# Performance work log

Hardware: AMD Instinct MI355X
Metric: run time of the kernel (lower is better)

## Reference

```python
import jax, jax.numpy as jnp
import numpy as np

HEADS = 8
EPS = 1e-6
LN_EPS = 1e-5


def avg_pool(x, k):
    b, c, h, w = x.shape
    return x.reshape(b, c, h // k, k, w // k, k).mean(axis=(3, 5))


def layernorm(x, g, b):
    mu = x.mean(-1, keepdims=True)
    var = x.var(-1, keepdims=True)
    return (x - mu) / jnp.sqrt(var + LN_EPS) * g + b


def pos_embed_2d(h, w, c):
    # original calls build_2d_sincos_position_embedding(w=h, h=w): grid over (h, w), row-major flatten
    gw, gh = jnp.meshgrid(jnp.arange(h, dtype=jnp.float32),
                          jnp.arange(w, dtype=jnp.float32), indexing='ij')
    pd = c // 4
    omega = 1.0 / (10000.0 ** (jnp.arange(pd, dtype=jnp.float32) / pd))
    ow = gw.reshape(-1, 1) * omega  # (h*w, pd)
    oh = gh.reshape(-1, 1) * omega
    return jnp.concatenate([jnp.sin(ow), jnp.cos(ow), jnp.sin(oh), jnp.cos(oh)], axis=1)  # (h*w, c)


def _forward(a3, a4, q_w, q_b, q_ln_g, q_ln_b, k_w, k_b, k_ln_g, k_ln_b,
             v_w, v_b, out_w, out_b, lin1_w, lin1_b, lin2_w, lin2_b,
             n1_g, n1_b, n2_g, n2_b, idx):
    orig_a3 = a3
    if idx == 2:
        a3d = avg_pool(a3, 2)
    else:
        a3d = avg_pool(a3, 4)
        a4 = avg_pool(a4, 2)
    bs, c, h, w = a3d.shape
    L = h * w  # tgt_len == src_len (a3_down and a4 have equal spatial size)
    hd = c // HEADS

    residual = a3d.reshape(bs, c, L).transpose(0, 2, 1)  # (b, L, c)
    x3 = residual
    x4 = a4.reshape(bs, c, L).transpose(0, 2, 1)
    pos = pos_embed_2d(h, w, c)  # (L, c)
    x3 = x3 + pos[None]
    x4 = x4 + pos[None]

    Q = layernorm(x3 @ q_w + q_b, q_ln_g, q_ln_b)
    K = layernorm(x4 @ k_w + k_b, k_ln_g, k_ln_b)
    V = x4 @ v_w + v_b
    Q = jax.nn.relu(Q).reshape(bs, L, HEADS, hd).transpose(0, 2, 1, 3)  # (b,h,L,d)
    K = jax.nn.relu(K).reshape(bs, L, HEADS, hd).transpose(0, 2, 1, 3)
    V = V.reshape(bs, L, HEADS, hd).transpose(0, 2, 1, 3)

    # cosFormer position reweighting: index = pi/2 * (1..m) / m
    m = L
    wi = (np.pi / 2.0) * jnp.arange(1, m + 1, dtype=jnp.float32) / m  # (m,)
    sn = jnp.sin(wi)[None, None, :, None]
    cs = jnp.cos(wi)[None, None, :, None]
    Q_ = jnp.concatenate([Q * sn, Q * cs], axis=-1)  # (b,h,L,2d)
    K_ = jnp.concatenate([K * sn, K * cs], axis=-1)

    KV = jnp.einsum('bhld,bhlm->bhdm', K_, V)                     # (b,h,2d,d)
    Z = 1.0 / jnp.maximum(jnp.einsum('bhld,bhd->bhl', Q_, K_.sum(axis=2)), EPS)
    attn = jnp.einsum('bhld,bhdm->bhlm', Q_, KV) * Z[..., None]   # (b,h,L,d)
    attn = attn.transpose(0, 2, 1, 3).reshape(bs, L, c)

    out = attn @ out_w + out_b
    out = layernorm(out, n1_g, n1_b)     # normalize_before=False -> norm1 applied
    out = residual + out                 # dropout=0
    res2 = out
    out = jax.nn.gelu(out @ lin1_w + lin1_b, approximate=False) @ lin2_w + lin2_b
    out = layernorm(out, n2_g, n2_b)
    out = res2 + out

    a3sa = out.transpose(0, 2, 1).reshape(bs, c, h, w)
    a3sa = jax.image.resize(a3sa, orig_a3.shape, method='bilinear')  # align_corners=False
    return a3sa * orig_a3


def setup_inputs() -> dict:
    key = jax.random.key(0)
    ks = jax.random.split(key, 10)
    B, C = 16, 256
    C4 = 4 * C

    def w(k, shp):
        return jax.random.normal(k, shp, dtype=jnp.float32) * 0.02

    return {
        'a3': jax.random.normal(ks[0], (B, C, 128, 128), dtype=jnp.float32),
        'a4': jax.random.normal(ks[1], (B, C, 64, 64), dtype=jnp.float32),
        'q_w': w(ks[2], (C, C)), 'q_b': jnp.zeros((C,), jnp.float32),
        'q_ln_g': jnp.ones((C,), jnp.float32), 'q_ln_b': jnp.zeros((C,), jnp.float32),
        'k_w': w(ks[3], (C, C)), 'k_b': jnp.zeros((C,), jnp.float32),
        'k_ln_g': jnp.ones((C,), jnp.float32), 'k_ln_b': jnp.zeros((C,), jnp.float32),
        'v_w': w(ks[4], (C, C)), 'v_b': jnp.zeros((C,), jnp.float32),
        'out_w': w(ks[5], (C, C)), 'out_b': jnp.zeros((C,), jnp.float32),
        'lin1_w': w(ks[6], (C, C4)), 'lin1_b': jnp.zeros((C4,), jnp.float32),
        'lin2_w': w(ks[7], (C4, C)), 'lin2_b': jnp.zeros((C,), jnp.float32),
        'n1_g': jnp.ones((C,), jnp.float32), 'n1_b': jnp.zeros((C,), jnp.float32),
        'n2_g': jnp.ones((C,), jnp.float32), 'n2_b': jnp.zeros((C,), jnp.float32),
        'idx': 2,
    }


def reference(a3, a4, q_w, q_b, q_ln_g, q_ln_b, k_w, k_b, k_ln_g, k_ln_b,
              v_w, v_b, out_w, out_b, lin1_w, lin1_b, lin2_w, lin2_b,
              n1_g, n1_b, n2_g, n2_b, idx):
    return _forward(a3, a4, q_w, q_b, q_ln_g, q_ln_b, k_w, k_b, k_ln_g, k_ln_b,
                    v_w, v_b, out_w, out_b, lin1_w, lin1_b, lin2_w, lin2_b,
                    n1_g, n1_b, n2_g, n2_b, idx)
```

## Files before the change

### kernel.cpp

```cpp
#include <hip/hip_runtime.h>
#include <hip/hip_bf16.h>
#include <math.h>

#define HEADS 8
#define LL 4096
#define CDIM 256
#define BATCH 16
#define NROWS (BATCH*LL)

typedef __attribute__((ext_vector_type(8))) __bf16 bf16x8;
typedef __attribute__((ext_vector_type(4))) float f32x4;

__device__ inline float b2f(ushort u) {
    union { unsigned u; float f; } v; v.u = ((unsigned)u) << 16; return v.f;
}
__device__ inline ushort f2b(float f) {
    union { float f; unsigned u; } v; v.f = f;
    unsigned r = (v.u + 0x7FFF + ((v.u >> 16) & 1)) >> 16;
    return (ushort)r;
}
__device__ inline void gload16(const void* g, void* l) {
    __builtin_amdgcn_global_load_lds(
        (const __attribute__((address_space(1))) unsigned int*)g,
        (__attribute__((address_space(3))) unsigned int*)l, 16, 0, 0);
}

__global__ __launch_bounds__(256) void prep_kernel(
    float* __restrict__ pos, float* __restrict__ snc,
    const float* __restrict__ q_w, const float* __restrict__ k_w,
    const float* __restrict__ v_w, const float* __restrict__ o_w,
    const float* __restrict__ w1, const float* __restrict__ w2,
    ushort* __restrict__ wqT, ushort* __restrict__ wkT,
    ushort* __restrict__ wvT, ushort* __restrict__ woT,
    ushort* __restrict__ w1T, ushort* __restrict__ w2T)
{
    __shared__ float t[32][33];
    int bid = blockIdx.x;
    int tid = threadIdx.x;
    if (bid < 1024) {
        int c = tid;
        int k = c & 63;
        float omega = expf(-(float)k * (9.210340371976184f / 64.0f));
        #pragma unroll
        for (int i = 0; i < 4; ++i) {
            int l = bid * 4 + i;
            int y = l >> 6, x = l & 63;
            float coord = (c < 128) ? (float)y : (float)x;
            float ang = coord * omega;
            float val = ((c & 127) < 64) ? sinf(ang) : cosf(ang);
            pos[l * CDIM + c] = val;
            if (c < 2) {
                float wi = 1.5707963267948966f * (float)(l + 1) / (float)LL;
                snc[l * 2 + c] = (c == 0) ? sinf(wi) : cosf(wi);
            }
        }
        return;
    }
    int id = bid - 1024;
    const float* W; ushort* Wt; int K, N, kb, nb;
    if (id < 64)       { W = q_w; Wt = wqT; K = 256;  N = 256;  kb = (id & 7) * 32;  nb = (id >> 3) * 32; }
    else if (id < 128) { id -= 64;  W = k_w; Wt = wkT; K = 256;  N = 256;  kb = (id & 7) * 32;  nb = (id >> 3) * 32; }
    else if (id < 192) { id -= 128; W = v_w; Wt = wvT; K = 256;  N = 256;  kb = (id & 7) * 32;  nb = (id >> 3) * 32; }
    else if (id < 256) { id -= 192; W = o_w; Wt = woT; K = 256;  N = 256;  kb = (id & 7) * 32;  nb = (id >> 3) * 32; }
    else if (id < 512) { id -= 256; W = w1;  Wt = w1T; K = 256;  N = 1024; kb = (id & 7) * 32;  nb = (id >> 3) * 32; }
    else               { id -= 512; W = w2;  Wt = w2T; K = 1024; N = 256;  kb = (id & 31) * 32; nb = (id >> 5) * 32; }
    int x = tid & 31, y = tid >> 5;
    #pragma unroll
    for (int i = 0; i < 4; ++i)
        t[y + i * 8][x] = W[(size_t)(kb + y + i * 8) * N + nb + x];
    __syncthreads();
    #pragma unroll
    for (int i = 0; i < 4; ++i) {
        int n = y + i * 8;
        Wt[(size_t)(nb + n) * K + kb + x] = f2b(t[x][n]);
    }
}

__global__ __launch_bounds__(256) void pool_x3_kernel(
    const float* __restrict__ a3, ushort* __restrict__ residual,
    ushort* __restrict__ x3b, const float* __restrict__ pos)
{
    __shared__ float raw[64][128];
    __shared__ float pooled[64][65];
    int i = blockIdx.x, ct = blockIdx.y, b = blockIdx.z;
    int tid = threadIdx.x;
    #pragma unroll
    for (int it = 0; it < 8; ++it) {
        int lin = (it * 256 + tid) * 4;
        int x = lin & 127;
        int cc = lin >> 7;
        size_t base = ((size_t)(b * 256 + ct * 64 + cc) * 128 + 2 * i) * 128 + x;
        float4 v0 = *(const float4*)&a3[base];
        float4 v1 = *(const float4*)&a3[base + 128];
        float4 s = make_float4(v0.x + v1.x, v0.y + v1.y, v0.z + v1.z, v0.w + v1.w);
        *(float4*)&raw[cc][x] = s;
    }
    __syncthreads();
    #pragma unroll
    for (int it = 0; it < 16; ++it) {
        int idx = it * 256 + tid;
        int j = idx & 63, cc = idx >> 6;
        pooled[cc][j] = 0.25f * (raw[cc][2 * j] + raw[cc][2 * j + 1]);
    }
    __syncthreads();
    #pragma unroll
    for (int it = 0; it < 16; ++it) {
        int cc = tid & 63;
        int jj = (tid >> 6) + it * 4;
        float val = pooled[cc][jj];
        int l = i * 64 + jj;
        int c = ct * 64 + cc;
        size_t o = (size_t)(b * LL + l) * CDIM + c;
        residual[o] = f2b(val);
        x3b[o] = f2b(val + pos[l * CDIM + c]);
    }
}

__global__ __launch_bounds__(256) void x4_kernel(
    const float* __restrict__ a4, ushort* __restrict__ x4b, const float* __restrict__ pos)
{
    __shared__ float t2[64][65];
    int y = blockIdx.x, ct = blockIdx.y, b = blockIdx.z, tid = threadIdx.x;
    #pragma unroll
    for (int it = 0; it < 16; ++it) {
        int idx = it * 256 + tid;
        int x = idx & 63, cc = idx >> 6;
        t2[cc][x] = a4[((size_t)(b * 256 + ct * 64 + cc) * 64 + y) * 64 + x];
    }
    __syncthreads();
    #pragma unroll
    for (int it = 0; it < 16; ++it) {
        int cc = tid & 63;
        int xx = (tid >> 6) + it * 4;
        int l = y * 64 + xx, c = ct * 64 + cc;
        x4b[(size_t)(b * LL + l) * CDIM + c] = f2b(t2[cc][xx] + pos[l * CDIM + c]);
    }
}

template<bool DO_LN, bool DO_RELU, bool DO_RES>
__global__ __launch_bounds__(256, 3) void gemm_mfma(
    const ushort* __restrict__ A, const ushort* __restrict__ Wt,
    const float* __restrict__ bias, const float* __restrict__ gam_,
    const float* __restrict__ bet_, const ushort* __restrict__ res,
    ushort* __restrict__ outb)
{
    __shared__ ushort As[2][64 * 32];
    __shared__ ushort Bs[2][256 * 32];
    __shared__ float redS[64][4];
    __shared__ float redQ[64][4];
    __shared__ float2 mustd[64];

    const int tid = threadIdx.x;
    const int lane = tid & 63;
    const int wv = tid >> 6;
    const int wvu = __builtin_amdgcn_readfirstlane(wv);
    const int row0 = blockIdx.x * 64;

    const int sr = tid >> 2;
    const int sg = (tid & 3) ^ ((sr >> 1) & 3);
    const ushort* aSrc = A + (size_t)(row0 + sr) * 256 + sg * 8;
    const ushort* bSrc = Wt + (size_t)sr * 256 + sg * 8;

    const int frSlot = (lane >> 4) ^ (((lane & 15) >> 1) & 3);

    f32x4 acc[4][4] = {};
    gload16(aSrc, (char*)&As[0][0] + wvu * 1024);
    #pragma unroll
    for (int j = 0; j < 4; ++j)
        gload16(bSrc + j * 64 * 256, (char*)&Bs[0][0] + j * 4096 + wvu * 1024);
    __syncthreads();

    int cur = 0;
    for (int t = 0; t < 8; ++t) {
        if (t < 7) {
            gload16(aSrc + (t + 1) * 32, (char*)&As[cur ^ 1][0] + wvu * 1024);
            #pragma unroll
            for (int j = 0; j < 4; ++j)
                gload16(bSrc + j * 64 * 256 + (t + 1) * 32,
                        (char*)&Bs[cur ^ 1][0] + j * 4096 + wvu * 1024);
        }
        bf16x8 af[4], bfr[4];
        #pragma unroll
        for (int f = 0; f < 4; ++f) {
            int r = f * 16 + (lane & 15);
            af[f] = *(const bf16x8*)&As[cur][r * 32 + frSlot * 8];
            int c = wv * 64 + f * 16 + (lane & 15);
            bfr[f] = *(const bf16x8*)&Bs[cur][c * 32 + frSlot * 8];
        }
        #pragma unroll
        for (int fi = 0; fi < 4; ++fi)
            #pragma unroll
            for (int fj = 0; fj < 4; ++fj)
                acc[fi][fj] = __builtin_amdgcn_mfma_f32_16x16x32_bf16(
                    af[fi], bfr[fj], acc[fi][fj], 0, 0, 0);
        __syncthreads();
        cur ^= 1;
    }

    const int cl = lane & 15;
    const int rg = lane >> 4;
    float bia[4], gmv[4], btv[4];
    #pragma unroll
    for (int fj = 0; fj < 4; ++fj) {
        int col = wv * 64 + fj * 16 + cl;
        bia[fj] = bias[col];
        if constexpr (DO_LN) { gmv[fj] = gam_[col]; btv[fj] = bet_[col]; }
    }
    #pragma unroll
    for (int fi = 0; fi < 4; ++fi)
        #pragma unroll
        for (int fj = 0; fj < 4; ++fj)
            #pragma unroll
            for (int j = 0; j < 4; ++j)
                acc[fi][fj][j] += bia[fj];

    if constexpr (DO_LN) {
        #pragma unroll
        for (int fi = 0; fi < 4; ++fi)
            #pragma unroll
            for (int j = 0; j < 4; ++j) {
                float s = acc[fi][0][j] + acc[fi][1][j] + acc[fi][2][j] + acc[fi][3][j];
                float q = acc[fi][0][j] * acc[fi][0][j] + acc[fi][1][j] * acc[fi][1][j]
                        + acc[fi][2][j] * acc[fi][2][j] + acc[fi][3][j] * acc[fi][3][j];
                #pragma unroll
                for (int m = 1; m <= 8; m <<= 1) {
                    s += __shfl_xor(s, m, 64);
                    q += __shfl_xor(q, m, 64);
                }
                if (cl == 0) { redS[fi * 16 + rg * 4 + j][wv] = s; redQ[fi * 16 + rg * 4 + j][wv] = q; }
            }
        __syncthreads();
        if (tid < 64) {
            float s = redS[tid][0] + redS[tid][1] + redS[tid][2] + redS[tid][3];
            float q = redQ[tid][0] + redQ[tid][1] + redQ[tid][2] + redQ[tid][3];
            float mu = s * (1.0f / 256.0f);
            float var = q * (1.0f / 256.0f) - mu * mu;
            mustd[tid] = make_float2(mu, rsqrtf(var + 1e-5f));
        }
        __syncthreads();
        #pragma unroll
        for (int fi = 0; fi < 4; ++fi)
            #pragma unroll
            for (int j = 0; j < 4; ++j) {
                float2 ms = mustd[fi * 16 + rg * 4 + j];
                #pragma unroll
                for (int fj = 0; fj < 4; ++fj)
                    acc[fi][fj][j] = (acc[fi][fj][j] - ms.x) * ms.y * gmv[fj] + btv[fj];
            }
    }
    if constexpr (DO_RELU) {
        #pragma unroll
        for (int fi = 0; fi < 4; ++fi)
            #pragma unroll
            for (int fj = 0; fj < 4; ++fj)
                #pragma unroll
                for (int j = 0; j < 4; ++j)
                    acc[fi][fj][j] = fmaxf(acc[fi][fj][j], 0.0f);
    }
    #pragma unroll
    for (int fi = 0; fi < 4; ++fi)
        #pragma unroll
        for (int j = 0; j < 4; ++j) {
            size_t row = row0 + fi * 16 + rg * 4 + j;
            size_t rbase = row * 256 + wv * 64 + cl;
            #pragma unroll
            for (int fj = 0; fj < 4; ++fj) {
                float v = acc[fi][fj][j];
                if constexpr (DO_RES) v += b2f(res[rbase + fj * 16]);
                outb[rbase + fj * 16] = f2b(v);
            }
        }
}

__global__ __launch_bounds__(256, 2) void mlp_fused(
    const ushort* __restrict__ res2, const ushort* __restrict__ w1T,
    const ushort* __restrict__ w2T, const float* __restrict__ b1,
    const float* __restrict__ b2, const float* __restrict__ gam_,
    const float* __restrict__ bet_, ushort* __restrict__ outb)
{
    __shared__ ushort As[2][64 * 32];
    __shared__ ushort Bs[2][256 * 32];
    __shared__ ushort h1c[64 * 256];
    __shared__ float redS[64][4];
    __shared__ float redQ[64][4];
    __shared__ float2 mustd[64];

    const int tid = threadIdx.x;
    const int lane = tid & 63;
    const int wv = tid >> 6;
    const int wvu = __builtin_amdgcn_readfirstlane(wv);
    const int row0 = blockIdx.x * 64;
    const int sr = tid >> 2;
    const int sg = (tid & 3) ^ ((sr >> 1) & 3);
    const ushort* aSrc = res2 + (size_t)(row0 + sr) * 256 + sg * 8;
    const int frSlot = (lane >> 4) ^ (((lane & 15) >> 1) & 3);
    const int cl = lane & 15;
    const int rg = lane >> 4;

    f32x4 acc2[4][4] = {};
    for (int c = 0; c < 4; ++c) {
        const ushort* b1Src = w1T + (size_t)(c * 256 + sr) * 256 + sg * 8;
        f32x4 acc1[4][4] = {};
        gload16(aSrc, (char*)&As[0][0] + wvu * 1024);
        #pragma unroll
        for (int j = 0; j < 4; ++j)
            gload16(b1Src + j * 64 * 256, (char*)&Bs[0][0] + j * 4096 + wvu * 1024);
        __syncthreads();
        int cur = 0;
        for (int t = 0; t < 8; ++t) {
            if (t < 7) {
                gload16(aSrc + (t + 1) * 32, (char*)&As[cur ^ 1][0] + wvu * 1024);
                #pragma unroll
                for (int j = 0; j < 4; ++j)
                    gload16(b1Src + j * 64 * 256 + (t + 1) * 32,
                            (char*)&Bs[cur ^ 1][0] + j * 4096 + wvu * 1024);
            }
            bf16x8 af[4], bfr[4];
            #pragma unroll
            for (int f = 0; f < 4; ++f) {
                int r = f * 16 + (lane & 15);
                af[f] = *(const bf16x8*)&As[cur][r * 32 + frSlot * 8];
                int cc2 = wv * 64 + f * 16 + (lane & 15);
                bfr[f] = *(const bf16x8*)&Bs[cur][cc2 * 32 + frSlot * 8];
            }
            #pragma unroll
            for (int fi = 0; fi < 4; ++fi)
                #pragma unroll
                for (int fj = 0; fj < 4; ++fj)
                    acc1[fi][fj] = __builtin_amdgcn_mfma_f32_16x16x32_bf16(
                        af[fi], bfr[fj], acc1[fi][fj], 0, 0, 0);
            __syncthreads();
            cur ^= 1;
        }
        float bia1[4];
        #pragma unroll
        for (int fj = 0; fj < 4; ++fj)
            bia1[fj] = b1[c * 256 + wv * 64 + fj * 16 + cl];
        #pragma unroll
        for (int fi = 0; fi < 4; ++fi)
            #pragma unroll
            for (int fj = 0; fj < 4; ++fj)
                #pragma unroll
                for (int j = 0; j < 4; ++j) {
                    float v = acc1[fi][fj][j] + bia1[fj];
                    float g = 0.5f * v * (1.0f + erff(v * 0.7071067811865476f));
                    int row = fi * 16 + rg * 4 + j;
                    int kk = wv * 64 + fj * 16 + cl;
                    int s_ = kk >> 5, gg = (kk >> 3) & 3, e = kk & 7;
                    int slot = gg ^ ((row >> 1) & 3);
                    h1c[row * 256 + s_ * 32 + slot * 8 + e] = f2b(g);
                }
        __syncthreads();
        const ushort* b2Src = w2T + (size_t)sr * 1024 + c * 256 + sg * 8;
        #pragma unroll
        for (int j = 0; j < 4; ++j)
            gload16(b2Src + (size_t)j * 64 * 1024, (char*)&Bs[0][0] + j * 4096 + wvu * 1024);
        __syncthreads();
        cur = 0;
        for (int t = 0; t < 8; ++t) {
            if (t < 7) {
                #pragma unroll
                for (int j = 0; j < 4; ++j)
                    gload16(b2Src + (size_t)j * 64 * 1024 + (t + 1) * 32,
                            (char*)&Bs[cur ^ 1][0] + j * 4096 + wvu * 1024);
            }
            bf16x8 af[4], bfr[4];
            #pragma unroll
            for (int f = 0; f < 4; ++f) {
                int r = f * 16 + (lane & 15);
                af[f] = *(const bf16x8*)&h1c[r * 256 + t * 32 + frSlot * 8];
                int cc2 = wv * 64 + f * 16 + (lane & 15);
                bfr[f] = *(const bf16x8*)&Bs[cur][cc2 * 32 + frSlot * 8];
            }
            #pragma unroll
            for (int fi = 0; fi < 4; ++fi)
                #pragma unroll
                for (int fj = 0; fj < 4; ++fj)
                    acc2[fi][fj] = __builtin_amdgcn_mfma_f32_16x16x32_bf16(
                        af[fi], bfr[fj], acc2[fi][fj], 0, 0, 0);
            __syncthreads();
            cur ^= 1;
        }
    }
    float bia[4], gmv[4], btv[4];
    #pragma unroll
    for (int fj = 0; fj < 4; ++fj) {
        int col = wv * 64 + fj * 16 + cl;
        bia[fj] = b2[col];
        gmv[fj] = gam_[col];
        btv[fj] = bet_[col];
    }
    #pragma unroll
    for (int fi = 0; fi < 4; ++fi)
        #pragma unroll
        for (int fj = 0; fj < 4; ++fj)
            #pragma unroll
            for (int j = 0; j < 4; ++j)
                acc2[fi][fj][j] += bia[fj];
    #pragma unroll
    for (int fi = 0; fi < 4; ++fi)
        #pragma unroll
        for (int j = 0; j < 4; ++j) {
            float s = acc2[fi][0][j] + acc2[fi][1][j] + acc2[fi][2][j] + acc2[fi][3][j];
            float q = acc2[fi][0][j] * acc2[fi][0][j] + acc2[fi][1][j] * acc2[fi][1][j]
                    + acc2[fi][2][j] * acc2[fi][2][j] + acc2[fi][3][j] * acc2[fi][3][j];
            #pragma unroll
            for (int m = 1; m <= 8; m <<= 1) {
                s += __shfl_xor(s, m, 64);
                q += __shfl_xor(q, m, 64);
            }
            if (cl == 0) { redS[fi * 16 + rg * 4 + j][wv] = s; redQ[fi * 16 + rg * 4 + j][wv] = q; }
        }
    __syncthreads();
    if (tid < 64) {
        float s = redS[tid][0] + redS[tid][1] + redS[tid][2] + redS[tid][3];
        float q = redQ[tid][0] + redQ[tid][1] + redQ[tid][2] + redQ[tid][3];
        float mu = s * (1.0f / 256.0f);
        float var = q * (1.0f / 256.0f) - mu * mu;
        mustd[tid] = make_float2(mu, rsqrtf(var + 1e-5f));
    }
    __syncthreads();
    #pragma unroll
    for (int fi = 0; fi < 4; ++fi)
        #pragma unroll
        for (int j = 0; j < 4; ++j) {
            float2 ms = mustd[fi * 16 + rg * 4 + j];
            size_t row = row0 + fi * 16 + rg * 4 + j;
            size_t rbase = row * 256 + wv * 64 + cl;
            #pragma unroll
            for (int fj = 0; fj < 4; ++fj) {
                float v = (acc2[fi][fj][j] - ms.x) * ms.y * gmv[fj] + btv[fj];
                v += b2f(res2[rbase + fj * 16]);
                outb[rbase + fj * 16] = f2b(v);
            }
        }
}

__global__ __launch_bounds__(256) void ksum_kernel(
    const ushort* __restrict__ Kmat, const float* __restrict__ snc,
    float* __restrict__ kspart)
{
    int ch = blockIdx.x, b = blockIdx.y;
    int c = threadIdx.x;
    int l0 = ch * 512;
    float as = 0.0f, ac = 0.0f;
    for (int i = 0; i < 512; ++i) {
        float k = b2f(Kmat[(size_t)(b * LL + l0 + i) * CDIM + c]);
        as += k * snc[(l0 + i) * 2];
        ac += k * snc[(l0 + i) * 2 + 1];
    }
    kspart[((size_t)(b * 8 + ch) * 2 + 0) * 256 + c] = as;
    kspart[((size_t)(b * 8 + ch) * 2 + 1) * 256 + c] = ac;
}

__global__ __launch_bounds__(256) void kv_kernel(
    const ushort* __restrict__ Kmat, const ushort* __restrict__ Vmat,
    const float* __restrict__ snc, float* __restrict__ kvpart)
{
    __shared__ float Kt[64][36];
    __shared__ float Vt[64][36];
    __shared__ float sns[64], css[64];
    int chunk = blockIdx.x;
    int bh = blockIdx.y;
    int b = bh >> 3, h = bh & 7;
    int tid = threadIdx.x;
    int m = tid & 31;
    int d0 = (tid >> 5) * 4;
    float accs[4] = {}, accc[4] = {};
    int l0chunk = chunk * 512;
    int lrow = tid >> 2;
    int lcol = (tid & 3) * 8;
    for (int sub = 0; sub < 8; ++sub) {
        int l0 = l0chunk + sub * 64;
        {
            size_t gbase = (size_t)(b * LL + l0 + lrow) * CDIM + h * 32 + lcol;
            uint4 kr = *(const uint4*)&Kmat[gbase];
            uint4 vr = *(const uint4*)&Vmat[gbase];
            float* kd = &Kt[lrow][lcol];
            float* vd = &Vt[lrow][lcol];
            kd[0] = b2f((ushort)(kr.x & 0xffff)); kd[1] = b2f((ushort)(kr.x >> 16));
            kd[2] = b2f((ushort)(kr.y & 0xffff)); kd[3] = b2f((ushort)(kr.y >> 16));
            kd[4] = b2f((ushort)(kr.z & 0xffff)); kd[5] = b2f((ushort)(kr.z >> 16));
            kd[6] = b2f((ushort)(kr.w & 0xffff)); kd[7] = b2f((ushort)(kr.w >> 16));
            vd[0] = b2f((ushort)(vr.x & 0xffff)); vd[1] = b2f((ushort)(vr.x >> 16));
            vd[2] = b2f((ushort)(vr.y & 0xffff)); vd[3] = b2f((ushort)(vr.y >> 16));
            vd[4] = b2f((ushort)(vr.z & 0xffff)); vd[5] = b2f((ushort)(vr.z >> 16));
            vd[6] = b2f((ushort)(vr.w & 0xffff)); vd[7] = b2f((ushort)(vr.w >> 16));
        }
        if (tid < 64) { sns[tid] = snc[(l0 + tid) * 2]; css[tid] = snc[(l0 + tid) * 2 + 1]; }
        __syncthreads();
        #pragma unroll 4
        for (int lt = 0; lt < 64; ++lt) {
            float v = Vt[lt][m];
            float vs = v * sns[lt];
            float vc = v * css[lt];
            float4 kd4 = *(const float4*)&Kt[lt][d0];
            accs[0] += kd4.x * vs; accc[0] += kd4.x * vc;
            accs[1] += kd4.y * vs; accc[1] += kd4.y * vc;
            accs[2] += kd4.z * vs; accc[2] += kd4.z * vc;
            accs[3] += kd4.w * vs; accc[3] += kd4.w * vc;
        }
        __syncthreads();
    }
    size_t base = (size_t)(bh * 8 + chunk) * 2048;
    #pragma unroll
    for (int i2 = 0; i2 < 4; ++i2) {
        kvpart[base + (d0 + i2) * 32 + m] = accs[i2];
        kvpart[base + 1024 + (d0 + i2) * 32 + m] = accc[i2];
    }
}

__global__ __launch_bounds__(256) void kvred_kernel(
    const float* __restrict__ kvpart, const float* __restrict__ kspart,
    ushort* __restrict__ Bimg)
{
    int bh = blockIdx.x;
    int b = bh >> 3, h = bh & 7;
    int tid = threadIdx.x;
    for (int e = tid; e < 2560; e += 256) {
        int n = e >> 5;
        int k = e & 31;
        int t = n >> 4, col = n & 15;
        float v = 0.0f;
        if (t < 4) {
            int off = (t >= 2 ? 1024 : 0) + k * 32 + (t & 1) * 16 + col;
            #pragma unroll
            for (int ch = 0; ch < 8; ++ch)
                v += kvpart[(size_t)(bh * 8 + ch) * 2048 + off];
        } else if (col < 2) {
            #pragma unroll
            for (int ch = 0; ch < 8; ++ch)
                v += kspart[((size_t)(b * 8 + ch) * 2 + col) * 256 + h * 32 + k];
        }
        ushort hi = f2b(v);
        ushort lo = f2b(v - b2f(hi));
        Bimg[(size_t)bh * 5120 + n * 32 + k] = hi;
        Bimg[(size_t)bh * 5120 + (80 + n) * 32 + k] = lo;
    }
}

__global__ __launch_bounds__(256, 2) void attn_mfma(
    const ushort* __restrict__ Qmat, const ushort* __restrict__ Bimg,
    const float* __restrict__ snc, ushort* __restrict__ attnOut)
{
    __shared__ ushort Bs[5120];
    int ltile = blockIdx.x, h = blockIdx.y, b = blockIdx.z;
    int bh = b * 8 + h;
    int tid = threadIdx.x;
    int lane = tid & 63;
    int wv = tid >> 6;

    for (int e = tid; e < 640; e += 256)
        *(uint4*)&Bs[e * 8] = *(const uint4*)&Bimg[(size_t)bh * 5120 + e * 8];
    __syncthreads();

    bf16x8 bfr[10];
    #pragma unroll
    for (int tt = 0; tt < 10; ++tt) {
        int row = (tt < 5 ? tt * 16 : 80 + (tt - 5) * 16) + (lane & 15);
        bfr[tt] = *(const bf16x8*)&Bs[row * 32 + (lane >> 4) * 8];
    }
    int lbase = ltile * 256 + wv * 64;
    bf16x8 af[4];
    #pragma unroll
    for (int fi = 0; fi < 4; ++fi) {
        int l = lbase + fi * 16 + (lane & 15);
        af[fi] = *(const bf16x8*)&Qmat[(size_t)(b * LL + l) * CDIM + h * 32 + (lane >> 4) * 8];
    }
    f32x4 acc[4][5] = {};
    #pragma unroll
    for (int fi = 0; fi < 4; ++fi)
        #pragma unroll
        for (int t = 0; t < 5; ++t) {
            acc[fi][t] = __builtin_amdgcn_mfma_f32_16x16x32_bf16(af[fi], bfr[t], acc[fi][t], 0, 0, 0);
            acc[fi][t] = __builtin_amdgcn_mfma_f32_16x16x32_bf16(af[fi], bfr[t + 5], acc[fi][t], 0, 0, 0);
        }

    int zlane = lane & 48;
    int cl = lane & 15;
    #pragma unroll
    for (int fi = 0; fi < 4; ++fi) {
        #pragma unroll
        for (int j = 0; j < 4; ++j) {
            float zraw = acc[fi][4][j];
            float zs = __shfl(zraw, zlane, 64);
            float zc = __shfl(zraw, zlane | 1, 64);
            int l = lbase + fi * 16 + ((lane >> 4) & 3) * 4 + j;
            float sn = snc[l * 2], cs = snc[l * 2 + 1];
            float den = sn * zs + cs * zc;
            float Z = 1.0f / fmaxf(den, 1e-6f);
            float v0 = (sn * acc[fi][0][j] + cs * acc[fi][2][j]) * Z;
            float v1 = (sn * acc[fi][1][j] + cs * acc[fi][3][j]) * Z;
            size_t ob = (size_t)(b * LL + l) * CDIM + h * 32 + cl;
            attnOut[ob] = f2b(v0);
            attnOut[ob + 16] = f2b(v1);
        }
    }
}

__global__ __launch_bounds__(256) void resize_mul_kernel(
    const ushort* __restrict__ ffeat, const float* __restrict__ a3, float* __restrict__ out)
{
    __shared__ float ft[3][64][65];
    int k = blockIdx.x, ct = blockIdx.y, b = blockIdx.z;
    int tid = threadIdx.x;
    for (int it = 0; it < 48; ++it) {
        int e = it * 256 + tid;
        int cc = e & 63;
        int xs = (e >> 6) & 63;
        int ys = e >> 12;
        int ysrc = min(max(k - 1 + ys, 0), 63);
        ft[ys][cc][xs] = b2f(ffeat[(size_t)(b * LL + ysrc * 64 + xs) * CDIM + ct * 64 + cc]);
    }
    __syncthreads();
    int x = tid & 127;
    int half = tid >> 7;
    int y = 2 * k + half;
    int ysA, ysB; float wyA, wyB;
    if (half == 0) { ysA = 0; ysB = 1; wyA = 0.25f; wyB = 0.75f; }
    else           { ysA = 1; ysB = 2; wyA = 0.75f; wyB = 0.25f; }
    int x0; float wx1;
    if ((x & 1) == 0) { x0 = x / 2 - 1; wx1 = 0.75f; }
    else              { x0 = x / 2;     wx1 = 0.25f; }
    int x0c = max(x0, 0);
    int x1c = min(x0 + 1, 63);
    float wx0 = 1.0f - wx1;
    for (int cc = 0; cc < 64; ++cc) {
        float rA = wx0 * ft[ysA][cc][x0c] + wx1 * ft[ysA][cc][x1c];
        float rB = wx0 * ft[ysB][cc][x0c] + wx1 * ft[ysB][cc][x1c];
        float val = wyA * rA + wyB * rB;
        size_t oidx = ((size_t)(b * 256 + ct * 64 + cc) * 128 + y) * 128 + x;
        out[oidx] = val * a3[oidx];
    }
}

extern "C" void kernel_launch(void* const* d_in, const int* in_sizes, int n_in,
                              void* d_out, int out_size, void* d_ws, size_t ws_size,
                              hipStream_t stream)
{
    const float* a3     = (const float*)d_in[0];
    const float* a4     = (const float*)d_in[1];
    const float* q_w    = (const float*)d_in[2];
    const float* q_b    = (const float*)d_in[3];
    const float* q_ln_g = (const float*)d_in[4];
    const float* q_ln_b = (const float*)d_in[5];
    const float* k_w    = (const float*)d_in[6];
    const float* k_b    = (const float*)d_in[7];
    const float* k_ln_g = (const float*)d_in[8];
    const float* k_ln_b = (const float*)d_in[9];
    const float* v_w    = (const float*)d_in[10];
    const float* v_b    = (const float*)d_in[11];
    const float* out_w  = (const float*)d_in[12];
    const float* out_b  = (const float*)d_in[13];
    const float* lin1_w = (const float*)d_in[14];
    const float* lin1_b = (const float*)d_in[15];
    const float* lin2_w = (const float*)d_in[16];
    const float* lin2_b = (const float*)d_in[17];
    const float* n1_g   = (const float*)d_in[18];
    const float* n1_b   = (const float*)d_in[19];
    const float* n2_g   = (const float*)d_in[20];
    const float* n2_b   = (const float*)d_in[21];
    float* out = (float*)d_out;
    char* base = (char*)d_ws;

    const size_t MiB = 1024 * 1024;
    float*  pos      = (float*)(base);
    float*  snc      = (float*)(base + 4 * MiB);
    ushort* wqT      = (ushort*)(base + 4 * MiB + 64 * 1024);
    ushort* wkT      = wqT + 256 * 256;
    ushort* wvT      = wkT + 256 * 256;
    ushort* woT      = wvT + 256 * 256;
    ushort* w1T      = woT + 256 * 256;
    ushort* w2T      = w1T + 1024 * 256;
    ushort* residual = (ushort*)(base + 6 * MiB);
    ushort* x3b      = (ushort*)(base + 38 * MiB);
    ushort* x4b      = (ushort*)(base + 70 * MiB);
    ushort* Qb       = (ushort*)(base + 102 * MiB);
    ushort* Kb       = (ushort*)(base + 134 * MiB);
    ushort* Vb       = (ushort*)(base + 166 * MiB);
    float*  kvp      = (float*)(base + 198 * MiB);
    float*  kspart   = (float*)(base + 206 * MiB);
    ushort* Bimg     = (ushort*)(base + 207 * MiB);
    ushort* attnb    = x3b;
    ushort* res2b    = x4b;
    ushort* ffeat    = residual;

    prep_kernel<<<1792, 256, 0, stream>>>(pos, snc, q_w, k_w, v_w, out_w, lin1_w, lin2_w,
                                          wqT, wkT, wvT, woT, w1T, w2T);
    pool_x3_kernel<<<dim3(64, 4, 16), 256, 0, stream>>>(a3, residual, x3b, pos);
    x4_kernel<<<dim3(64, 4, 16), 256, 0, stream>>>(a4, x4b, pos);

    gemm_mfma<true, true, false><<<NROWS / 64, 256, 0, stream>>>(
        x3b, wqT, q_b, q_ln_g, q_ln_b, nullptr, Qb);
    gemm_mfma<true, true, false><<<NROWS / 64, 256, 0, stream>>>(
        x4b, wkT, k_b, k_ln_g, k_ln_b, nullptr, Kb);
    gemm_mfma<false, false, false><<<NROWS / 64, 256, 0, stream>>>(
        x4b, wvT, v_b, nullptr, nullptr, nullptr, Vb);

    ksum_kernel<<<dim3(8, 16), 256, 0, stream>>>(Kb, snc, kspart);
    kv_kernel<<<dim3(8, 128), 256, 0, stream>>>(Kb, Vb, snc, kvp);
    kvred_kernel<<<128, 256, 0, stream>>>(kvp, kspart, Bimg);
    attn_mfma<<<dim3(16, 8, 16), 256, 0, stream>>>(Qb, Bimg, snc, attnb);

    gemm_mfma<true, false, true><<<NROWS / 64, 256, 0, stream>>>(
        attnb, woT, out_b, n1_g, n1_b, residual, res2b);
    mlp_fused<<<NROWS / 64, 256, 0, stream>>>(
        res2b, w1T, w2T, lin1_b, lin2_b, n2_g, n2_b, ffeat);

    resize_mul_kernel<<<dim3(64, 4, 16), 256, 0, stream>>>(ffeat, a3, out);
}
```

Measured before the change: 608.8 us.

## Fuse K/V projections with K-sum reduction and pipeline MLP weight loads

Merges the K and V projection GEMMs into one kernel that reads the x4 tile once, and folds the sin/cos-weighted K column sums into its epilogue through atomics into a buffer zeroed by an extra prep block. This removes the separate ksum pass over K. The MLP kernel also prefetches the next stage's weight tile across chunk boundaries to avoid pipeline restarts, and switches the hidden buffer to a padded per-chunk layout. The costs are more LDS and registers in the fused GEMM, which may lower occupancy, and float atomics that make the K sums order-nondeterministic.

Result: faster. 564.0 us (-7.4%).

```diff
diff --git a/kernel.cpp b/kernel.cpp
--- a/kernel.cpp
+++ b/kernel.cpp
@@ -9,6 +9,7 @@
 #define NROWS (BATCH*LL)
 
 typedef __attribute__((ext_vector_type(8))) __bf16 bf16x8;
+typedef __attribute__((ext_vector_type(4))) __bf16 bf16x4;
 typedef __attribute__((ext_vector_type(4))) float f32x4;
 
 __device__ inline float b2f(ushort u) {
@@ -32,11 +33,16 @@
     const float* __restrict__ w1, const float* __restrict__ w2,
     ushort* __restrict__ wqT, ushort* __restrict__ wkT,
     ushort* __restrict__ wvT, ushort* __restrict__ woT,
-    ushort* __restrict__ w1T, ushort* __restrict__ w2T)
+    ushort* __restrict__ w1T, ushort* __restrict__ w2T,
+    float* __restrict__ ksglob)
 {
     __shared__ float t[32][33];
     int bid = blockIdx.x;
     int tid = threadIdx.x;
+    if (bid == 1792) {
+        for (int i = tid; i < BATCH * 2 * 256; i += 256) ksglob[i] = 0.0f;
+        return;
+    }
     if (bid < 1024) {
         int c = tid;
         int k = c & 63;
@@ -272,6 +278,167 @@
         }
 }
 
+__global__ __launch_bounds__(256, 2) void gemm_kv(
+    const ushort* __restrict__ A, const ushort* __restrict__ wkT,
+    const ushort* __restrict__ wvT, const float* __restrict__ k_b,
+    const float* __restrict__ k_g, const float* __restrict__ k_beta,
+    const float* __restrict__ v_b, const float* __restrict__ snc,
+    float* __restrict__ ksglob, ushort* __restrict__ Kb, ushort* __restrict__ Vb)
+{
+    __shared__ ushort As[2][64 * 32];
+    __shared__ ushort BsK[2][256 * 32];
+    __shared__ ushort BsV[2][256 * 32];
+    __shared__ float redS[64][4];
+    __shared__ float redQ[64][4];
+    __shared__ float2 mustd[64];
+
+    const int tid = threadIdx.x;
+    const int lane = tid & 63;
+    const int wv = tid >> 6;
+    const int wvu = __builtin_amdgcn_readfirstlane(wv);
+    const int row0 = blockIdx.x * 64;
+
+    const int sr = tid >> 2;
+    const int sg = (tid & 3) ^ ((sr >> 1) & 3);
+    const ushort* aSrc = A + (size_t)(row0 + sr) * 256 + sg * 8;
+    const ushort* bkSrc = wkT + (size_t)sr * 256 + sg * 8;
+    const ushort* bvSrc = wvT + (size_t)sr * 256 + sg * 8;
+
+    const int frSlot = (lane >> 4) ^ (((lane & 15) >> 1) & 3);
+
+    f32x4 accK[4][4] = {};
+    f32x4 accV[4][4] = {};
+    gload16(aSrc, (char*)&As[0][0] + wvu * 1024);
+    #pragma unroll
+    for (int j = 0; j < 4; ++j) {
+        gload16(bkSrc + j * 64 * 256, (char*)&BsK[0][0] + j * 4096 + wvu * 1024);
+        gload16(bvSrc + j * 64 * 256, (char*)&BsV[0][0] + j * 4096 + wvu * 1024);
+    }
+    __syncthreads();
+
+    int cur = 0;
+    for (int t = 0; t < 8; ++t) {
+        if (t < 7) {
+            gload16(aSrc + (t + 1) * 32, (char*)&As[cur ^ 1][0] + wvu * 1024);
+            #pragma unroll
+            for (int j = 0; j < 4; ++j) {
+                gload16(bkSrc + j * 64 * 256 + (t + 1) * 32,
+                        (char*)&BsK[cur ^ 1][0] + j * 4096 + wvu * 1024);
+                gload16(bvSrc + j * 64 * 256 + (t + 1) * 32,
+                        (char*)&BsV[cur ^ 1][0] + j * 4096 + wvu * 1024);
+            }
+        }
+        bf16x8 af[4], bk[4], bv[4];
+        #pragma unroll
+        for (int f = 0; f < 4; ++f) {
+            int r = f * 16 + (lane & 15);
+            af[f] = *(const bf16x8*)&As[cur][r * 32 + frSlot * 8];
+            int c = wv * 64 + f * 16 + (lane & 15);
+            bk[f] = *(const bf16x8*)&BsK[cur][c * 32 + frSlot * 8];
+            bv[f] = *(const bf16x8*)&BsV[cur][c * 32 + frSlot * 8];
+        }
+        #pragma unroll
+        for (int fi = 0; fi < 4; ++fi)
+            #pragma unroll
+            for (int fj = 0; fj < 4; ++fj) {
+                accK[fi][fj] = __builtin_amdgcn_mfma_f32_16x16x32_bf16(
+                    af[fi], bk[fj], accK[fi][fj], 0, 0, 0);
+                accV[fi][fj] = __builtin_amdgcn_mfma_f32_16x16x32_bf16(
+                    af[fi], bv[fj], accV[fi][fj], 0, 0, 0);
+            }
+        __syncthreads();
+        cur ^= 1;
+    }
+
+    const int cl = lane & 15;
+    const int rg = lane >> 4;
+    #pragma unroll
+    for (int fj = 0; fj < 4; ++fj) {
+        float bv_ = v_b[wv * 64 + fj * 16 + cl];
+        #pragma unroll
+        for (int fi = 0; fi < 4; ++fi)
+            #pragma unroll
+            for (int j = 0; j < 4; ++j)
+                accV[fi][fj][j] += bv_;
+    }
+    #pragma unroll
+    for (int fi = 0; fi < 4; ++fi)
+        #pragma unroll
+        for (int j = 0; j < 4; ++j) {
+            size_t rbase = (size_t)(row0 + fi * 16 + rg * 4 + j) * 256 + wv * 64 + cl;
+            #pragma unroll
+            for (int fj = 0; fj < 4; ++fj)
+                Vb[rbase + fj * 16] = f2b(accV[fi][fj][j]);
+        }
+    float bia[4], gmv[4], btv[4];
+    #pragma unroll
+    for (int fj = 0; fj < 4; ++fj) {
+        int col = wv * 64 + fj * 16 + cl;
+        bia[fj] = k_b[col]; gmv[fj] = k_g[col]; btv[fj] = k_beta[col];
+    }
+    #pragma unroll
+    for (int fi = 0; fi < 4; ++fi)
+        #pragma unroll
+        for (int fj = 0; fj < 4; ++fj)
+            #pragma unroll
+            for (int j = 0; j < 4; ++j)
+                accK[fi][fj][j] += bia[fj];
+    #pragma unroll
+    for (int fi = 0; fi < 4; ++fi)
+        #pragma unroll
+        for (int j = 0; j < 4; ++j) {
+            float s = accK[fi][0][j] + accK[fi][1][j] + accK[fi][2][j] + accK[fi][3][j];
+            float q = accK[fi][0][j] * accK[fi][0][j] + accK[fi][1][j] * accK[fi][1][j]
+                    + accK[fi][2][j] * accK[fi][2][j] + accK[fi][3][j] * accK[fi][3][j];
+            #pragma unroll
+            for (int m = 1; m <= 8; m <<= 1) {
+                s += __shfl_xor(s, m, 64);
+                q += __shfl_xor(q, m, 64);
+            }
+            if (cl == 0) { redS[fi * 16 + rg * 4 + j][wv] = s; redQ[fi * 16 + rg * 4 + j][wv] = q; }
+        }
+    __syncthreads();
+    if (tid < 64) {
+        float s = redS[tid][0] + redS[tid][1] + redS[tid][2] + redS[tid][3];
+        float q = redQ[tid][0] + redQ[tid][1] + redQ[tid][2] + redQ[tid][3];
+        float mu = s * (1.0f / 256.0f);
+        float var = q * (1.0f / 256.0f) - mu * mu;
+        mustd[tid] = make_float2(mu, rsqrtf(var + 1e-5f));
+    }
+    __syncthreads();
+    float kss[4] = {}, ksc[4] = {};
+    #pragma unroll
+    for (int fi = 0; fi < 4; ++fi)
+        #pragma unroll
+        for (int j = 0; j < 4; ++j) {
+            int rloc = fi * 16 + rg * 4 + j;
+            float2 ms = mustd[rloc];
+            int l = (row0 + rloc) & (LL - 1);
+            float sn = snc[l * 2], cs = snc[l * 2 + 1];
+            size_t rbase = (size_t)(row0 + rloc) * 256 + wv * 64 + cl;
+            #pragma unroll
+            for (int fj = 0; fj < 4; ++fj) {
+                float v = (accK[fi][fj][j] - ms.x) * ms.y * gmv[fj] + btv[fj];
+                v = fmaxf(v, 0.0f);
+                Kb[rbase + fj * 16] = f2b(v);
+                kss[fj] += sn * v;
+                ksc[fj] += cs * v;
+            }
+        }
+    int b = row0 >> 12;
+    #pragma unroll
+    for (int fj = 0; fj < 4; ++fj) {
+        float s = kss[fj], c = ksc[fj];
+        s += __shfl_xor(s, 16, 64); s += __shfl_xor(s, 32, 64);
+        c += __shfl_xor(c, 16, 64); c += __shfl_xor(c, 32, 64);
+        if (rg == 0) {
+            int col = wv * 64 + fj * 16 + cl;
+            atomicAdd(&ksglob[((size_t)b * 2 + 0) * 256 + col], s);
+            atomicAdd(&ksglob[((size_t)b * 2 + 1) * 256 + col], c);
+        }
+    }
+}
+
 __global__ __launch_bounds__(256, 2) void mlp_fused(
     const ushort* __restrict__ res2, const ushort* __restrict__ w1T,
     const ushort* __restrict__ w2T, const float* __restrict__ b1,
@@ -280,7 +447,7 @@
 {
     __shared__ ushort As[2][64 * 32];
     __shared__ ushort Bs[2][256 * 32];
-    __shared__ ushort h1c[64 * 256];
+    __shared__ ushort h1c[8 * 64 * 36];
     __shared__ float redS[64][4];
     __shared__ float redQ[64][4];
     __shared__ float2 mustd[64];
@@ -298,21 +465,30 @@
     const int rg = lane >> 4;
 
     f32x4 acc2[4][4] = {};
+    gload16(aSrc, (char*)&As[0][0] + wvu * 1024);
+    #pragma unroll
+    for (int j = 0; j < 4; ++j)
+        gload16(w1T + (size_t)(j * 64 + sr) * 256 + sg * 8,
+                (char*)&Bs[0][0] + j * 4096 + wvu * 1024);
+    __syncthreads();
+    int cur = 0;
+
     for (int c = 0; c < 4; ++c) {
         const ushort* b1Src = w1T + (size_t)(c * 256 + sr) * 256 + sg * 8;
+        const ushort* b2Src = w2T + (size_t)sr * 1024 + c * 256 + sg * 8;
         f32x4 acc1[4][4] = {};
-        gload16(aSrc, (char*)&As[0][0] + wvu * 1024);
-        #pragma unroll
-        for (int j = 0; j < 4; ++j)
-            gload16(b1Src + j * 64 * 256, (char*)&Bs[0][0] + j * 4096 + wvu * 1024);
-        __syncthreads();
-        int cur = 0;
         for (int t = 0; t < 8; ++t) {
             if (t < 7) {
                 gload16(aSrc + (t + 1) * 32, (char*)&As[cur ^ 1][0] + wvu * 1024);
                 #pragma unroll
                 for (int j = 0; j < 4; ++j)
                     gload16(b1Src + j * 64 * 256 + (t + 1) * 32,
+                            (char*)&Bs[cur ^ 1][0] + j * 4096 + wvu * 1024);
+            } else {
+                gload16(aSrc, (char*)&As[cur ^ 1][0] + wvu * 1024);
+                #pragma unroll
+                for (int j = 0; j < 4; ++j)
+                    gload16(b2Src + (size_t)j * 64 * 1024,
                             (char*)&Bs[cur ^ 1][0] + j * 4096 + wvu * 1024);
             }
             bf16x8 af[4], bfr[4];
@@ -339,36 +515,42 @@
         #pragma unroll
         for (int fi = 0; fi < 4; ++fi)
             #pragma unroll
-            for (int fj = 0; fj < 4; ++fj)
+            for (int fj = 0; fj < 4; ++fj) {
+                int tch = wv * 2 + (fj >> 1);
+                int kk_local = (fj & 1) * 16 + cl;
                 #pragma unroll
                 for (int j = 0; j < 4; ++j) {
                     float v = acc1[fi][fj][j] + bia1[fj];
                     float g = 0.5f * v * (1.0f + erff(v * 0.7071067811865476f));
                     int row = fi * 16 + rg * 4 + j;
-                    int kk = wv * 64 + fj * 16 + cl;
-                    int s_ = kk >> 5, gg = (kk >> 3) & 3, e = kk & 7;
-                    int slot = gg ^ ((row >> 1) & 3);
-                    h1c[row * 256 + s_ * 32 + slot * 8 + e] = f2b(g);
+                    h1c[tch * 2304 + row * 36 + kk_local] = f2b(g);
                 }
+            }
         __syncthreads();
-        const ushort* b2Src = w2T + (size_t)sr * 1024 + c * 256 + sg * 8;
-        #pragma unroll
-        for (int j = 0; j < 4; ++j)
-            gload16(b2Src + (size_t)j * 64 * 1024, (char*)&Bs[0][0] + j * 4096 + wvu * 1024);
-        __syncthreads();
-        cur = 0;
         for (int t = 0; t < 8; ++t) {
             if (t < 7) {
                 #pragma unroll
                 for (int j = 0; j < 4; ++j)
                     gload16(b2Src + (size_t)j * 64 * 1024 + (t + 1) * 32,
                             (char*)&Bs[cur ^ 1][0] + j * 4096 + wvu * 1024);
+            } else {
+                int cn = (c < 3) ? c + 1 : 3;
+                #pragma unroll
+                for (int j = 0; j < 4; ++j)
+                    gload16(w1T + (size_t)(cn * 256 + j * 64 + sr) * 256 + sg * 8,
+                            (char*)&Bs[cur ^ 1][0] + j * 4096 + wvu * 1024);
             }
             bf16x8 af[4], bfr[4];
             #pragma unroll
             for (int f = 0; f < 4; ++f) {
                 int r = f * 16 + (lane & 15);
-                af[f] = *(const bf16x8*)&h1c[r * 256 + t * 32 + frSlot * 8];
+                int ho = t * 2304 + r * 36 + (lane >> 4) * 8;
+                bf16x4 lo = *(const bf16x4*)&h1c[ho];
+                bf16x4 hi = *(const bf16x4*)&h1c[ho + 4];
+                bf16x8 a_;
+                a_[0] = lo[0]; a_[1] = lo[1]; a_[2] = lo[2]; a_[3] = lo[3];
+                a_[4] = hi[0]; a_[5] = hi[1]; a_[6] = hi[2]; a_[7] = hi[3];
+                af[f] = a_;
                 int cc2 = wv * 64 + f * 16 + (lane & 15);
                 bfr[f] = *(const bf16x8*)&Bs[cur][cc2 * 32 + frSlot * 8];
             }
@@ -434,23 +616,6 @@
                 outb[rbase + fj * 16] = f2b(v);
             }
         }
-}
-
-__global__ __launch_bounds__(256) void ksum_kernel(
-    const ushort* __restrict__ Kmat, const float* __restrict__ snc,
-    float* __restrict__ kspart)
-{
-    int ch = blockIdx.x, b = blockIdx.y;
-    int c = threadIdx.x;
-    int l0 = ch * 512;
-    float as = 0.0f, ac = 0.0f;
-    for (int i = 0; i < 512; ++i) {
-        float k = b2f(Kmat[(size_t)(b * LL + l0 + i) * CDIM + c]);
-        as += k * snc[(l0 + i) * 2];
-        ac += k * snc[(l0 + i) * 2 + 1];
-    }
-    kspart[((size_t)(b * 8 + ch) * 2 + 0) * 256 + c] = as;
-    kspart[((size_t)(b * 8 + ch) * 2 + 1) * 256 + c] = ac;
 }
 
 __global__ __launch_bounds__(256) void kv_kernel(
@@ -511,7 +676,7 @@
 }
 
 __global__ __launch_bounds__(256) void kvred_kernel(
-    const float* __restrict__ kvpart, const float* __restrict__ kspart,
+    const float* __restrict__ kvpart, const float* __restrict__ ksglob,
     ushort* __restrict__ Bimg)
 {
     int bh = blockIdx.x;
@@ -528,9 +693,7 @@
             for (int ch = 0; ch < 8; ++ch)
                 v += kvpart[(size_t)(bh * 8 + ch) * 2048 + off];
         } else if (col < 2) {
-            #pragma unroll
-            for (int ch = 0; ch < 8; ++ch)
-                v += kspart[((size_t)(b * 8 + ch) * 2 + col) * 256 + h * 32 + k];
+            v = ksglob[((size_t)b * 2 + col) * 256 + h * 32 + k];
         }
         ushort hi = f2b(v);
         ushort lo = f2b(v - b2f(hi));
@@ -679,27 +842,24 @@
     ushort* Kb       = (ushort*)(base + 134 * MiB);
     ushort* Vb       = (ushort*)(base + 166 * MiB);
     float*  kvp      = (float*)(base + 198 * MiB);
-    float*  kspart   = (float*)(base + 206 * MiB);
+    float*  ksglob   = (float*)(base + 206 * MiB);
     ushort* Bimg     = (ushort*)(base + 207 * MiB);
     ushort* attnb    = x3b;
     ushort* res2b    = x4b;
     ushort* ffeat    = residual;
 
-    prep_kernel<<<1792, 256, 0, stream>>>(pos, snc, q_w, k_w, v_w, out_w, lin1_w, lin2_w,
-                                          wqT, wkT, wvT, woT, w1T, w2T);
+    prep_kernel<<<1793, 256, 0, stream>>>(pos, snc, q_w, k_w, v_w, out_w, lin1_w, lin2_w,
+                                          wqT, wkT, wvT, woT, w1T, w2T, ksglob);
     pool_x3_kernel<<<dim3(64, 4, 16), 256, 0, stream>>>(a3, residual, x3b, pos);
     x4_kernel<<<dim3(64, 4, 16), 256, 0, stream>>>(a4, x4b, pos);
 
     gemm_mfma<true, true, false><<<NROWS / 64, 256, 0, stream>>>(
         x3b, wqT, q_b, q_ln_g, q_ln_b, nullptr, Qb);
-    gemm_mfma<true, true, false><<<NROWS / 64, 256, 0, stream>>>(
-        x4b, wkT, k_b, k_ln_g, k_ln_b, nullptr, Kb);
-    gemm_mfma<false, false, false><<<NROWS / 64, 256, 0, stream>>>(
-        x4b, wvT, v_b, nullptr, nullptr, nullptr, Vb);
-
-    ksum_kernel<<<dim3(8, 16), 256, 0, stream>>>(Kb, snc, kspart);
+    gemm_kv<<<NROWS / 64, 256, 0, stream>>>(
+        x4b, wkT, wvT, k_b, k_ln_g, k_ln_b, v_b, snc, ksglob, Kb, Vb);
+
     kv_kernel<<<dim3(8, 128), 256, 0, stream>>>(Kb, Vb, snc, kvp);
-    kvred_kernel<<<128, 256, 0, stream>>>(kvp, kspart, Bimg);
+    kvred_kernel<<<128, 256, 0, stream>>>(kvp, ksglob, Bimg);
     attn_mfma<<<dim3(16, 8, 16), 256, 0, stream>>>(Qb, Bimg, snc, attnb);
 
     gemm_mfma<true, false, true><<<NROWS / 64, 256, 0, stream>>>(
```
